# Kernel optimization log

Hardware: AMD Instinct MI355X
Metric: run time of the kernel (lower is better)

The kernel has to match this reference:

```python
import jax, jax.numpy as jnp
import numpy as np

B, S, E, H = 2, 2048, 1024, 16
D = E // H  # head_dim = 64

def setup_inputs() -> dict:
    key = jax.random.key(0)
    ks = jax.random.split(key, 11)
    s = 1.0 / np.sqrt(E)
    inp = {
        'query': jax.random.normal(ks[0], (B, S, E), jnp.float32),
        'key':   jax.random.normal(ks[1], (B, S, E), jnp.float32),
        'value': jax.random.normal(ks[2], (B, S, E), jnp.float32),
        'Wq': jax.random.uniform(ks[3], (E, E), jnp.float32, -s, s),
        'bq': jax.random.uniform(ks[4], (E,), jnp.float32, -s, s),
        'Wk': jax.random.uniform(ks[5], (E, E), jnp.float32, -s, s),
        'bk': jax.random.uniform(ks[6], (E,), jnp.float32, -s, s),
        'Wv': jax.random.uniform(ks[7], (E, E), jnp.float32, -s, s),
        'bv': jax.random.uniform(ks[8], (E,), jnp.float32, -s, s),
        'Wo': jax.random.uniform(ks[9], (E, E), jnp.float32, -s, s),
        'bo': jax.random.uniform(ks[10], (E,), jnp.float32, -s, s),
    }
    return inp

def reference(query, key, value, Wq, bq, Wk, bk, Wv, bv, Wo, bo):
    # project and split heads: [B,S,E] -> [B,H,S,D]
    def proj(x, W, b):
        y = jnp.einsum('bse,fe->bsf', x, W) + b  # torch Linear: x @ W.T + b
        return y.reshape(B, S, H, D).transpose(0, 2, 1, 3)
    q = proj(query, Wq, bq)
    k = proj(key, Wk, bk)
    v = proj(value, Wv, bv)
    scores = jnp.einsum('bhqd,bhkd->bhqk', q, k) / jnp.sqrt(jnp.float32(D))
    attn = jax.nn.softmax(scores, axis=-1)
    out = jnp.einsum('bhqk,bhkd->bhqd', attn, v)  # [B,H,S,D]
    out = out.transpose(0, 2, 1, 3).reshape(B, S, E)
    return jnp.einsum('bse,fe->bsf', out, Wo) + bo
```

## Files before the change

kernel.cpp:

```cpp
#include <hip/hip_runtime.h>

#define B_ 2
#define S_ 2048
#define E_ 1024
#define H_ 16
#define D_ 64
#define M_ (B_*S_)
#define K_ E_

typedef __attribute__((ext_vector_type(8))) short  short8;
typedef __attribute__((ext_vector_type(4))) float  f32x4;
typedef __attribute__((ext_vector_type(8))) unsigned short u16x8;
typedef __attribute__((ext_vector_type(4))) unsigned short u16x4;
typedef __attribute__((ext_vector_type(4))) unsigned int   u32x4;

#define QSCALE 0.18033688011112042f

__device__ __forceinline__ unsigned short f2bf(float f) {
    unsigned u = __float_as_uint(f);
    u += 0x7fffu + ((u >> 16) & 1u);
    return (unsigned short)(u >> 16);
}

__device__ __forceinline__ void gl_lds16(const ushort* g, ushort* l) {
    __builtin_amdgcn_global_load_lds((const __attribute__((address_space(1))) void*)g,
                                     (__attribute__((address_space(3))) void*)l,
                                     16, 0, 0);
}

__global__ __launch_bounds__(256)
void cvt_all(const float* __restrict__ q, const float* __restrict__ k,
             const float* __restrict__ v, const float* __restrict__ wq,
             const float* __restrict__ wk, const float* __restrict__ wv,
             const float* __restrict__ wo, ushort* __restrict__ dst)
{
    const int bid = blockIdx.x;
    const float* src;
    size_t dof;
    int local;
    if (bid < 6144) {
        const int t = bid >> 11;
        src = (t == 0) ? q : (t == 1) ? k : v;
        dof = (size_t)t * 4194304u;
        local = bid & 2047;
    } else {
        const int r = bid - 6144;
        const int t = r >> 9;
        src = (t == 0) ? wq : (t == 1) ? wk : (t == 2) ? wv : wo;
        dof = 12582912u + (size_t)t * 1048576u;
        local = r & 511;
    }
    const size_t idx = (size_t)local * 2048 + threadIdx.x * 8;
    const float4 a = *(const float4*)(src + idx);
    const float4 b = *(const float4*)(src + idx + 4);
    u16x8 o;
    o[0] = f2bf(a.x); o[1] = f2bf(a.y); o[2] = f2bf(a.z); o[3] = f2bf(a.w);
    o[4] = f2bf(b.x); o[5] = f2bf(b.y); o[6] = f2bf(b.z); o[7] = f2bf(b.w);
    *(u16x8*)(dst + dof + idx) = o;
}

template<int SWAP>
__device__ __forceinline__ void gemm_core(const ushort* __restrict__ X,
                                          const ushort* __restrict__ W,
                                          int m0, int n0,
                                          f32x4 acc[4][4],
                                          ushort* Ast, ushort* Bst)
{
    const int tid  = threadIdx.x;
    const int lane = tid & 63;
    const int w    = tid >> 6;
    const int wm   = w & 1, wn = w >> 1;
    const int r0   = tid >> 2;
    const int c8   = (tid & 3) * 8;

    const f32x4 zero = {0.f, 0.f, 0.f, 0.f};
    #pragma unroll
    for (int mt = 0; mt < 4; ++mt)
        #pragma unroll
        for (int nt = 0; nt < 4; ++nt) acc[mt][nt] = zero;

    const int kb = (lane >> 4) * 8;

    for (int k0 = 0; k0 < K_; k0 += 32) {
        __syncthreads();
        const ushort* ga = X + (size_t)(m0 + r0) * K_ + k0 + c8;
        gl_lds16(ga, Ast + tid * 8);
        gl_lds16(ga + (size_t)64 * K_, Ast + 2048 + tid * 8);
        const ushort* gb = W + (size_t)(n0 + r0) * K_ + k0 + c8;
        gl_lds16(gb, Bst + tid * 8);
        gl_lds16(gb + (size_t)64 * K_, Bst + 2048 + tid * 8);
        __syncthreads();

        short8 af[4], bf[4];
        #pragma unroll
        for (int mt = 0; mt < 4; ++mt)
            af[mt] = *(const short8*)(Ast + (wm * 64 + mt * 16 + (lane & 15)) * 32 + kb);
        #pragma unroll
        for (int nt = 0; nt < 4; ++nt)
            bf[nt] = *(const short8*)(Bst + (wn * 64 + nt * 16 + (lane & 15)) * 32 + kb);
        #pragma unroll
        for (int mt = 0; mt < 4; ++mt)
            #pragma unroll
            for (int nt = 0; nt < 4; ++nt) {
                if (SWAP)
                    acc[mt][nt] = __builtin_amdgcn_mfma_f32_16x16x32_bf16(bf[nt], af[mt], acc[mt][nt], 0, 0, 0);
                else
                    acc[mt][nt] = __builtin_amdgcn_mfma_f32_16x16x32_bf16(af[mt], bf[nt], acc[mt][nt], 0, 0, 0);
            }
    }
}

__global__ __launch_bounds__(256)
void gemm_qkv(const ushort* __restrict__ Xq, const ushort* __restrict__ Xk,
              const ushort* __restrict__ Xv, const ushort* __restrict__ Wq,
              const ushort* __restrict__ Wk, const ushort* __restrict__ Wv,
              const float* __restrict__ bq, const float* __restrict__ bk,
              const float* __restrict__ bv, ushort* __restrict__ Qh,
              ushort* __restrict__ Kh, ushort* __restrict__ Vt)
{
    __shared__ ushort Ast[128 * 32];
    __shared__ ushort Bst[128 * 32];
    const int z = blockIdx.z;
    const ushort* X = (z == 0) ? Xq : (z == 1) ? Xk : Xv;
    const ushort* W = (z == 0) ? Wq : (z == 1) ? Wk : Wv;
    const float* bias = (z == 0) ? bq : (z == 1) ? bk : bv;
    ushort* dst = (z == 0) ? Qh : (z == 1) ? Kh : Vt;

    const int m0 = blockIdx.y * 128, n0 = blockIdx.x * 128;
    f32x4 acc[4][4];
    const int lane = threadIdx.x & 63, w = threadIdx.x >> 6;
    const int wm = w & 1, wn = w >> 1;
    const int l15 = lane & 15, quad = lane >> 4;

    if (z < 2) {
        gemm_core<1>(X, W, m0, n0, acc, Ast, Bst);
        const float qsc = (z == 0) ? QSCALE : 1.0f;
        #pragma unroll
        for (int nt = 0; nt < 4; ++nt) {
            const int nb = n0 + wn * 64 + nt * 16 + quad * 4;
            const int h = nb >> 6, d0 = nb & 63;
            const float4 b4 = *(const float4*)(bias + nb);
            const float bb4[4] = {b4.x, b4.y, b4.z, b4.w};
            #pragma unroll
            for (int mt = 0; mt < 4; ++mt) {
                const int tok = m0 + wm * 64 + mt * 16 + l15;
                const int b = tok >> 11, s = tok & (S_ - 1);
                u16x4 pk;
                #pragma unroll
                for (int r = 0; r < 4; ++r)
                    pk[r] = f2bf((acc[mt][nt][r] + bb4[r]) * qsc);
                *(u16x4*)&dst[(((size_t)(b * H_ + h) * S_) + s) * D_ + d0] = pk;
            }
        }
    } else {
        gemm_core<0>(X, W, m0, n0, acc, Ast, Bst);
        float bias4[4];
        #pragma unroll
        for (int nt = 0; nt < 4; ++nt)
            bias4[nt] = bias[n0 + wn * 64 + nt * 16 + l15];
        #pragma unroll
        for (int mt = 0; mt < 4; ++mt) {
            const int mrow0 = m0 + wm * 64 + mt * 16 + (quad * 4);
            const int b = mrow0 >> 11;
            const int s0 = mrow0 & (S_ - 1);
            #pragma unroll
            for (int nt = 0; nt < 4; ++nt) {
                const int n = n0 + wn * 64 + nt * 16 + l15;
                const int h = n >> 6, d = n & 63;
                u16x4 pk;
                #pragma unroll
                for (int r = 0; r < 4; ++r) pk[r] = f2bf(acc[mt][nt][r] + bias4[nt]);
                *(u16x4*)&Vt[(((size_t)(b * H_ + h) * D_) + d) * S_ + s0] = pk;
            }
        }
    }
}

__global__ __launch_bounds__(256)
void gemm_out(const ushort* __restrict__ X, const ushort* __restrict__ W,
              const float* __restrict__ bias, float* __restrict__ out)
{
    __shared__ ushort Ast[128 * 32];
    __shared__ ushort Bst[128 * 32];
    const int m0 = blockIdx.y * 128, n0 = blockIdx.x * 128;
    f32x4 acc[4][4];
    gemm_core<0>(X, W, m0, n0, acc, Ast, Bst);

    const int lane = threadIdx.x & 63, w = threadIdx.x >> 6;
    const int wm = w & 1, wn = w >> 1;
    float bias4[4];
    #pragma unroll
    for (int nt = 0; nt < 4; ++nt)
        bias4[nt] = bias[n0 + wn * 64 + nt * 16 + (lane & 15)];

    #pragma unroll
    for (int mt = 0; mt < 4; ++mt) {
        const int mrow0 = m0 + wm * 64 + mt * 16 + ((lane >> 4) * 4);
        #pragma unroll
        for (int nt = 0; nt < 4; ++nt) {
            const int n = n0 + wn * 64 + nt * 16 + (lane & 15);
            #pragma unroll
            for (int r = 0; r < 4; ++r)
                out[(size_t)(mrow0 + r) * E_ + n] = acc[mt][nt][r] + bias4[nt];
        }
    }
}

#define NTILE (S_ / 64)
__global__ __launch_bounds__(256, 2)
void flash_mfma(const ushort* __restrict__ Qg, const ushort* __restrict__ Kg,
                const ushort* __restrict__ Vg, ushort* __restrict__ AO)
{
    __shared__ ushort sh[20480];
    ushort* Qs = sh;

    const int tid = threadIdx.x, lane = tid & 63, w = tid >> 6;
    const int l15 = lane & 15, quad = lane >> 4;
    const int q0 = blockIdx.x * 64, h = blockIdx.y, b = blockIdx.z;
    const size_t qk_off = (size_t)(b * H_ + h) * S_ * D_;
    const size_t vt_off = (size_t)(b * H_ + h) * D_ * S_;

    #pragma unroll
    for (int i = 0; i < 2; ++i) {
        const int chunk = w + i * 4;
        const int row = chunk * 8 + (lane >> 3);
        const int gcol = (lane & 7) ^ (row & 7);
        gl_lds16(Qg + qk_off + (size_t)(q0 + row) * D_ + gcol * 8,
                 Qs + chunk * 512 + lane * 8);
        gl_lds16(Kg + qk_off + (size_t)row * D_ + gcol * 8,
                 sh + 4096 + chunk * 512 + lane * 8);
        gl_lds16(Vg + vt_off + (size_t)row * S_ + gcol * 8,
                 sh + 8192 + chunk * 512 + lane * 8);
    }
    __syncthreads();

    short8 qb[4][2];
    #pragma unroll
    for (int g = 0; g < 4; ++g)
        #pragma unroll
        for (int kt = 0; kt < 2; ++kt)
            qb[g][kt] = *(const short8*)&Qs[(g * 16 + l15) * 64 +
                                            (((kt * 4 + quad) ^ (l15 & 7)) * 8)];

    const f32x4 zero = {0.f, 0.f, 0.f, 0.f};
    f32x4 o[4][4];
    #pragma unroll
    for (int g = 0; g < 4; ++g)
        #pragma unroll
        for (int nt = 0; nt < 4; ++nt) o[g][nt] = zero;
    float lsum[4] = {0.f, 0.f, 0.f, 0.f};

    for (int jt = 0; jt < NTILE; ++jt) {
        ushort* Kc = sh + 4096 + (jt & 1) * 8192;
        ushort* Vc = Kc + 4096;

        short8 ka[2];
        #pragma unroll
        for (int kt = 0; kt < 2; ++kt)
            ka[kt] = *(const short8*)&Kc[(w * 16 + l15) * 64 +
                                         (((kt * 4 + quad) ^ (l15 & 7)) * 8)];
        const int gidx = (2 * w + (quad >> 1)) ^ (l15 & 7);
        uint2 vv[4];
        #pragma unroll
        for (int nt = 0; nt < 4; ++nt)
            vv[nt] = *(const uint2*)&Vc[(nt * 16 + l15) * 64 + gidx * 8 + (quad & 1) * 4];

        if (jt + 1 < NTILE) {
            const int j0n = (jt + 1) * 64;
            ushort* Kn = sh + 4096 + ((jt + 1) & 1) * 8192;
            ushort* Vn = Kn + 4096;
            #pragma unroll
            for (int i = 0; i < 2; ++i) {
                const int chunk = w + i * 4;
                const int row = chunk * 8 + (lane >> 3);
                const int gcol = (lane & 7) ^ (row & 7);
                gl_lds16(Kg + qk_off + (size_t)(j0n + row) * D_ + gcol * 8,
                         Kn + chunk * 512 + lane * 8);
                gl_lds16(Vg + vt_off + (size_t)row * S_ + j0n + gcol * 8,
                         Vn + chunk * 512 + lane * 8);
            }
        }

        f32x4 t[4];
        #pragma unroll
        for (int g = 0; g < 4; ++g) {
            t[g] = __builtin_amdgcn_mfma_f32_16x16x32_bf16(ka[0], qb[g][0], zero, 0, 0, 0);
            t[g] = __builtin_amdgcn_mfma_f32_16x16x32_bf16(ka[1], qb[g][1], t[g], 0, 0, 0);
        }

        short8 pa8[4];
        #pragma unroll
        for (int g = 0; g < 4; ++g) {
            const float p0 = exp2f(t[g][0]), p1 = exp2f(t[g][1]);
            const float p2 = exp2f(t[g][2]), p3 = exp2f(t[g][3]);
            lsum[g] += (p0 + p1) + (p2 + p3);
            const unsigned a0 = __float_as_uint(p0) + 0x8000u;
            const unsigned a1 = __float_as_uint(p1) + 0x8000u;
            const unsigned a2 = __float_as_uint(p2) + 0x8000u;
            const unsigned a3 = __float_as_uint(p3) + 0x8000u;
            u32x4 pk;
            pk[0] = (a1 & 0xffff0000u) | (a0 >> 16);
            pk[1] = (a3 & 0xffff0000u) | (a2 >> 16);
            pk[2] = 0u;
            pk[3] = 0u;
            pa8[g] = __builtin_bit_cast(short8, pk);
        }

        #pragma unroll
        for (int nt = 0; nt < 4; ++nt) {
            u32x4 vk;
            vk[0] = vv[nt].x; vk[1] = vv[nt].y; vk[2] = vv[nt].x; vk[3] = vv[nt].y;
            const short8 vb8 = __builtin_bit_cast(short8, vk);
            #pragma unroll
            for (int g = 0; g < 4; ++g)
                o[g][nt] = __builtin_amdgcn_mfma_f32_16x16x32_bf16(pa8[g], vb8, o[g][nt], 0, 0, 0);
        }

        __syncthreads();
    }

    #pragma unroll
    for (int g = 0; g < 4; ++g) {
        lsum[g] += __shfl_xor(lsum[g], 16);
        lsum[g] += __shfl_xor(lsum[g], 32);
    }
    __syncthreads();
    float* fb = (float*)sh;
    #pragma unroll
    for (int g = 0; g < 4; ++g) {
        if (w != g) {
            #pragma unroll
            for (int nt = 0; nt < 4; ++nt)
                #pragma unroll
                for (int r = 0; r < 4; ++r)
                    fb[w * 1024 + (nt * 4 + r) * 64 + lane] = o[g][nt][r];
            if (quad == 0) fb[4096 + w * 64 + l15] = lsum[g];
        }
        __syncthreads();
        if (w == g) {
            #pragma unroll
            for (int ws = 0; ws < 4; ++ws) {
                if (ws == g) continue;
                #pragma unroll
                for (int nt = 0; nt < 4; ++nt)
                    #pragma unroll
                    for (int r = 0; r < 4; ++r)
                        o[g][nt][r] += fb[ws * 1024 + (nt * 4 + r) * 64 + lane];
                lsum[g] += fb[4096 + ws * 64 + l15];
            }
        }
        __syncthreads();
    }

    #pragma unroll
    for (int g = 0; g < 4; ++g) {
        if (w == g) {
            const float inv = 1.0f / lsum[g];
            float invr[4];
            #pragma unroll
            for (int r = 0; r < 4; ++r)
                invr[r] = __shfl(inv, (lane & 0x30) | (quad * 4 + r));
            #pragma unroll
            for (int nt = 0; nt < 4; ++nt) {
                const int e = h * 64 + nt * 16 + l15;
                #pragma unroll
                for (int r = 0; r < 4; ++r) {
                    const int s = q0 + g * 16 + quad * 4 + r;
                    AO[(size_t)(b * S_ + s) * E_ + e] = f2bf(o[g][nt][r] * invr[r]);
                }
            }
        }
    }
}

extern "C" void kernel_launch(void* const* d_in, const int* in_sizes, int n_in,
                              void* d_out, int out_size, void* d_ws, size_t ws_size,
                              hipStream_t stream) {
    const float* query = (const float*)d_in[0];
    const float* key   = (const float*)d_in[1];
    const float* value = (const float*)d_in[2];
    const float* Wq = (const float*)d_in[3];
    const float* bq = (const float*)d_in[4];
    const float* Wk = (const float*)d_in[5];
    const float* bk = (const float*)d_in[6];
    const float* Wv = (const float*)d_in[7];
    const float* bv = (const float*)d_in[8];
    const float* Wo = (const float*)d_in[9];
    const float* bo = (const float*)d_in[10];
    float* out = (float*)d_out;

    ushort* ws = (ushort*)d_ws;
    ushort* Xq  = ws;
    ushort* Xk  = ws + 4194304u;
    ushort* Xv  = ws + 8388608u;
    ushort* Wqb = ws + 12582912u;
    ushort* Wkb = ws + 13631488u;
    ushort* Wvb = ws + 14680064u;
    ushort* Wob = ws + 15728640u;
    ushort* Qh  = ws + 16777216u;
    ushort* Kh  = ws + 20971520u;
    ushort* Vt  = ws + 25165824u;
    ushort* AO  = ws + 29360128u;

    cvt_all<<<8192, 256, 0, stream>>>(query, key, value, Wq, Wk, Wv, Wo, ws);
    gemm_qkv<<<dim3(8, 32, 3), 256, 0, stream>>>(Xq, Xk, Xv, Wqb, Wkb, Wvb,
                                                 bq, bk, bv, Qh, Kh, Vt);
    flash_mfma<<<dim3(32, 16, 2), 256, 0, stream>>>(Qh, Kh, Vt, AO);
    gemm_out<<<dim3(8, 32, 1), 256, 0, stream>>>(AO, Wob, bo, out);
}
```

Baseline: 256.9 us.

## Give each wave private K/V LDS slices and drop per-tile block barrier

Each wave now loads only the K rows and V columns it consumes into its own double-buffered LDS region, laid out in MFMA fragment order. The per-iteration __syncthreads is replaced by a per-wave vmcnt wait plus a scheduling barrier, so waves no longer stall on each other. The aim is to remove block-wide synchronization and simplify LDS addressing. The risk is correctness: a wave issues the prefetch into the other buffer while its own earlier reads of that buffer may still be in flight, and the hard-coded waitcnt value may not cover the async global-to-LDS loads correctly.

```diff
diff --git a/kernel.cpp b/kernel.cpp
--- a/kernel.cpp
+++ b/kernel.cpp
@@ -219,6 +219,9 @@
     const int q0 = blockIdx.x * 64, h = blockIdx.y, b = blockIdx.z;
     const size_t qk_off = (size_t)(b * H_ + h) * S_ * D_;
     const size_t vt_off = (size_t)(b * H_ + h) * D_ * S_;
+    const ushort* Kh_ = Kg + qk_off;
+    const ushort* Vh_ = Vg + vt_off;
+    ushort* Wbase = sh + 4096 + w * 4096;
 
     #pragma unroll
     for (int i = 0; i < 2; ++i) {
@@ -227,10 +230,18 @@
         const int gcol = (lane & 7) ^ (row & 7);
         gl_lds16(Qg + qk_off + (size_t)(q0 + row) * D_ + gcol * 8,
                  Qs + chunk * 512 + lane * 8);
-        gl_lds16(Kg + qk_off + (size_t)row * D_ + gcol * 8,
-                 sh + 4096 + chunk * 512 + lane * 8);
-        gl_lds16(Vg + vt_off + (size_t)row * S_ + gcol * 8,
-                 sh + 8192 + chunk * 512 + lane * 8);
+    }
+    {
+        ushort* Kb = Wbase;
+        ushort* Vb = Wbase + 1024;
+        #pragma unroll
+        for (int kt = 0; kt < 2; ++kt)
+            gl_lds16(Kh_ + (size_t)(w * 16 + l15) * D_ + kt * 32 + quad * 8,
+                     Kb + kt * 512 + lane * 8);
+        #pragma unroll
+        for (int i = 0; i < 2; ++i)
+            gl_lds16(Vh_ + (size_t)(i * 32 + (lane >> 1)) * S_ + w * 16 + (lane & 1) * 8,
+                     Vb + i * 512 + lane * 8);
     }
     __syncthreads();
 
@@ -251,35 +262,34 @@
     float lsum[4] = {0.f, 0.f, 0.f, 0.f};
 
     for (int jt = 0; jt < NTILE; ++jt) {
-        ushort* Kc = sh + 4096 + (jt & 1) * 8192;
-        ushort* Vc = Kc + 4096;
-
-        short8 ka[2];
-        #pragma unroll
-        for (int kt = 0; kt < 2; ++kt)
-            ka[kt] = *(const short8*)&Kc[(w * 16 + l15) * 64 +
-                                         (((kt * 4 + quad) ^ (l15 & 7)) * 8)];
-        const int gidx = (2 * w + (quad >> 1)) ^ (l15 & 7);
-        uint2 vv[4];
-        #pragma unroll
-        for (int nt = 0; nt < 4; ++nt)
-            vv[nt] = *(const uint2*)&Vc[(nt * 16 + l15) * 64 + gidx * 8 + (quad & 1) * 4];
+        ushort* Kc = Wbase + (jt & 1) * 2048;
+        ushort* Vc = Kc + 1024;
+
+        __builtin_amdgcn_s_waitcnt(0x0F70);
+        __builtin_amdgcn_sched_barrier(0);
 
         if (jt + 1 < NTILE) {
             const int j0n = (jt + 1) * 64;
-            ushort* Kn = sh + 4096 + ((jt + 1) & 1) * 8192;
-            ushort* Vn = Kn + 4096;
-            #pragma unroll
-            for (int i = 0; i < 2; ++i) {
-                const int chunk = w + i * 4;
-                const int row = chunk * 8 + (lane >> 3);
-                const int gcol = (lane & 7) ^ (row & 7);
-                gl_lds16(Kg + qk_off + (size_t)(j0n + row) * D_ + gcol * 8,
-                         Kn + chunk * 512 + lane * 8);
-                gl_lds16(Vg + vt_off + (size_t)row * S_ + j0n + gcol * 8,
-                         Vn + chunk * 512 + lane * 8);
-            }
-        }
+            ushort* Kn = Wbase + ((jt + 1) & 1) * 2048;
+            ushort* Vn = Kn + 1024;
+            #pragma unroll
+            for (int kt = 0; kt < 2; ++kt)
+                gl_lds16(Kh_ + (size_t)(j0n + w * 16 + l15) * D_ + kt * 32 + quad * 8,
+                         Kn + kt * 512 + lane * 8);
+            #pragma unroll
+            for (int i = 0; i < 2; ++i)
+                gl_lds16(Vh_ + (size_t)(i * 32 + (lane >> 1)) * S_ + j0n + w * 16 + (lane & 1) * 8,
+                         Vn + i * 512 + lane * 8);
+        }
+
+        short8 ka[2];
+        #pragma unroll
+        for (int kt = 0; kt < 2; ++kt)
+            ka[kt] = *(const short8*)&Kc[kt * 512 + lane * 8];
+        uint2 vv[4];
+        #pragma unroll
+        for (int nt = 0; nt < 4; ++nt)
+            vv[nt] = *(const uint2*)&Vc[(nt * 16 + l15) * 16 + quad * 4];
 
         f32x4 t[4];
         #pragma unroll
@@ -315,8 +325,6 @@
             for (int g = 0; g < 4; ++g)
                 o[g][nt] = __builtin_amdgcn_mfma_f32_16x16x32_bf16(pa8[g], vb8, o[g][nt], 0, 0, 0);
         }
-
-        __syncthreads();
     }
 
     #pragma unroll
```

Result: no change. 257.3 us (+0.2%).
